# Kernel optimization log

Measured on AMD Instinct MI355X. Metric: run time of the kernel, lower is better.

The kernel has to match this reference:

```python
import jax, jax.numpy as jnp
import numpy as np

N_NODES = 100000
N_EDGES = 1600000
D_IN = 128
D_OUT = 128


def setup_inputs() -> dict:
    key = jax.random.key(0)
    ks = jax.random.split(key, 7)
    x = jax.random.normal(ks[0], (N_NODES, D_IN), dtype=jnp.float32)
    edge_index = jax.random.randint(ks[1], (2, N_EDGES), 0, N_NODES, dtype=jnp.int64)
    edge_weights = jax.random.uniform(ks[2], (N_EDGES,), dtype=jnp.float32)
    s = 1.0 / np.sqrt(D_IN)
    W_lin = jax.random.uniform(ks[3], (D_IN, D_OUT), minval=-s, maxval=s, dtype=jnp.float32)
    b_lin = jax.random.uniform(ks[4], (D_OUT,), minval=-s, maxval=s, dtype=jnp.float32)
    W_agg = jax.random.uniform(ks[5], (D_IN, D_OUT), minval=-s, maxval=s, dtype=jnp.float32)
    b_agg = jax.random.uniform(ks[6], (D_OUT,), minval=-s, maxval=s, dtype=jnp.float32)
    return {"x": x, "edge_index": edge_index, "edge_weights": edge_weights,
            "W_lin": W_lin, "b_lin": b_lin, "W_agg": W_agg, "b_agg": b_agg}


def reference(x, edge_index, edge_weights, W_lin, b_lin, W_agg, b_agg):
    # self transform: [N, D_out]
    self_features = x @ W_lin + b_lin
    row, col = edge_index[0], edge_index[1]
    # gather neighbor features along edges: [E, D_in]
    neighbor_features = x[col] * edge_weights[:, None]
    # per-edge transform: [E, D_out]
    msgs = neighbor_features @ W_agg + b_agg
    # scatter-add to destination nodes (index_add_ on row)
    aggregated = jax.ops.segment_sum(msgs, row, num_segments=x.shape[0])
    return self_features + aggregated
```

## Files before the change

kernel.cpp:

```cpp
#include <hip/hip_runtime.h>

#define N_NODES 100000
#define N_EDGES 1600000
#define D 128
#define SCAN_CHUNK 1024
#define NB_SCAN ((N_NODES + SCAN_CHUNK - 1) / SCAN_CHUNK)

#define BSHIFT 9
#define BUCK_NODES 512
#define NBUCK 196
#define SCAP 10240
#define PART_CHUNK 4096
#define PART_BLOCKS ((N_EDGES + PART_CHUNK - 1) / PART_CHUNK)
#define CONV_BLOCKS 6250
#define W_BLOCKS 128

typedef __attribute__((ext_vector_type(8))) short bf16x8;
typedef __attribute__((ext_vector_type(4))) float f32x4;
typedef __attribute__((ext_vector_type(4))) unsigned u32x4;

__device__ __forceinline__ unsigned bf16rne(float f) {
  unsigned u = __float_as_uint(f);
  return (u + 0x7fffu + ((u >> 16) & 1u)) >> 16;
}

#define T5_OFF    200
#define T5_FRAGW  100304
#define T5_SRT    116688
#define T5_XH     3316688
#define T5_ZH     9718736
#define WS_T5_BYTES ((size_t)16120784 * 4)

#define WS_OFF   100000
#define WS_BSUM  200004
#define WS_SRT   200192
#define WS_XH    3400192
#define WS_T1_BYTES ((size_t)3400192 * 4)
#define WS_T2_BYTES ((size_t)(3400192 + 6400000) * 4)

__global__ __launch_bounds__(256) void part_kernel(
    const int* __restrict__ ei, const float* __restrict__ ew,
    const float* __restrict__ x,
    const float* __restrict__ Wl, const float* __restrict__ Wa,
    int* __restrict__ pcur, int2* __restrict__ stage,
    uint4* __restrict__ xh4, unsigned short* __restrict__ fragW) {
  __shared__ int cntL[256];
  __shared__ int s0[256];
  __shared__ int gb[NBUCK];
  __shared__ int curL[NBUCK];
  __shared__ int2 recL[PART_CHUNK];
  __shared__ unsigned char buckL[PART_CHUNK];
  int bid = blockIdx.x, tid = threadIdx.x;

  if (bid < PART_BLOCKS) {
    cntL[tid] = 0;
    __syncthreads();
    int e0 = bid * PART_CHUNK;
    int tot = min(PART_CHUNK, N_EDGES - e0);
#pragma unroll
    for (int k = 0; k < PART_CHUNK / 256; k++) {
      int e = e0 + k * 256 + tid;
      if (e < N_EDGES) atomicAdd(&cntL[ei[e] >> BSHIFT], 1);
    }
    __syncthreads();
    s0[tid] = cntL[tid];
    __syncthreads();
    for (int o = 1; o < 256; o <<= 1) {
      int add = (tid >= o) ? s0[tid - o] : 0;
      __syncthreads();
      s0[tid] += add;
      __syncthreads();
    }
    if (tid < NBUCK) {
      gb[tid] = atomicAdd(&pcur[tid], cntL[tid]);
      curL[tid] = 0;
    }
    __syncthreads();
#pragma unroll
    for (int k = 0; k < PART_CHUNK / 256; k++) {
      int e = e0 + k * 256 + tid;
      if (e < N_EDGES) {
        int d = ei[e];
        int src = ei[N_EDGES + e];
        float w = ew[e];
        int b = d >> BSHIFT;
        int r = atomicAdd(&curL[b], 1);
        int slot = (s0[b] - cntL[b]) + r;
        recL[slot] = make_int2(src | ((d & (BUCK_NODES - 1)) << 17),
                               __float_as_int(w));
        buckL[slot] = (unsigned char)b;
      }
    }
    __syncthreads();
    for (int i = tid; i < tot; i += 256) {
      int b = buckL[i];
      int idx = gb[b] + (i - (s0[b] - cntL[b]));
      stage[(size_t)b * SCAP + idx] = recL[i];
    }
  } else if (bid < PART_BLOCKS + CONV_BLOCKS) {
    int g = (bid - PART_BLOCKS) * 256 + tid;
    const u32x4* xp = reinterpret_cast<const u32x4*>(x);
    u32x4 a = __builtin_nontemporal_load(xp + (size_t)g * 2);
    u32x4 b = __builtin_nontemporal_load(xp + (size_t)g * 2 + 1);
    uint4 o;
    o.x = bf16rne(__uint_as_float(a.x)) | (bf16rne(__uint_as_float(a.y)) << 16);
    o.y = bf16rne(__uint_as_float(a.z)) | (bf16rne(__uint_as_float(a.w)) << 16);
    o.z = bf16rne(__uint_as_float(b.x)) | (bf16rne(__uint_as_float(b.y)) << 16);
    o.w = bf16rne(__uint_as_float(b.z)) | (bf16rne(__uint_as_float(b.w)) << 16);
    xh4[g] = o;
  } else {
    int tau = (bid - PART_BLOCKS - CONV_BLOCKS) * 256 + tid;
    int slot = tau >> 3, j = tau & 7;
    int lane = slot & 63, ft = slot >> 6;
    int t = ft & 7, s = ft >> 3;
    int kl = (s & 3) * 32 + (lane >> 4) * 8 + j;
    int n = t * 16 + (lane & 15);
    float v = (s < 4 ? Wl : Wa)[kl * 128 + n];
    fragW[slot * 8 + j] = (unsigned short)bf16rne(v);
  }
}

__global__ __launch_bounds__(512) void binB2_kernel(const int* __restrict__ pcur,
                                                    const int2* __restrict__ stage,
                                                    int* __restrict__ off,
                                                    int2* __restrict__ srt) {
  __shared__ int pc[NBUCK];
  __shared__ int sa[BUCK_NODES];
  __shared__ int sb[BUCK_NODES];
  __shared__ int curL[BUCK_NODES];
  __shared__ int baseS, mS;
  int b = blockIdx.x, tid = threadIdx.x;
  if (tid < NBUCK) pc[tid] = pcur[tid];
  if (tid < BUCK_NODES) sa[tid] = 0;
  __syncthreads();
  if (tid == 0) {
    int s = 0;
    for (int i = 0; i < b; i++) s += pc[i];
    baseS = s;
    mS = pc[b];
  }
  __syncthreads();
  int base = baseS, m = mS;
  const int2* sp = stage + (size_t)b * SCAP;
  for (int r = tid; r < m; r += 512)
    atomicAdd(&sa[((unsigned)sp[r].x) >> 17], 1);
  __syncthreads();
  int* srcb = sa;
  int* dstb = sb;
  for (int o = 1; o < BUCK_NODES; o <<= 1) {
    if (tid < BUCK_NODES)
      dstb[tid] = srcb[tid] + (tid >= o ? srcb[tid - o] : 0);
    __syncthreads();
    int* t = srcb; srcb = dstb; dstb = t;
  }
  int nb = b << BSHIFT;
  int nn = min(BUCK_NODES, N_NODES - nb);
  if (tid < BUCK_NODES) {
    int ex = tid ? srcb[tid - 1] : 0;
    curL[tid] = ex;
    if (tid < nn) off[nb + tid] = base + ex;
  }
  if (tid == 0 && b == NBUCK - 1) off[N_NODES] = base + srcb[nn - 1];
  __syncthreads();
  for (int r = tid; r < m; r += 512) {
    int2 rec = sp[r];
    int ldst = ((unsigned)rec.x) >> 17;
    int s = atomicAdd(&curL[ldst], 1);
    srt[base + s] = make_int2(rec.x & 0x1FFFF, rec.y);
  }
}

#define FACC(s_, p_, w_)                                                    \
  {                                                                         \
    acc1[s_][0] = fmaf(w_, __uint_as_float((p_).x << 16), acc1[s_][0]);     \
    acc1[s_][1] = fmaf(w_, __uint_as_float((p_).x & 0xffff0000u), acc1[s_][1]); \
    acc1[s_][2] = fmaf(w_, __uint_as_float((p_).y << 16), acc1[s_][2]);     \
    acc1[s_][3] = fmaf(w_, __uint_as_float((p_).y & 0xffff0000u), acc1[s_][3]); \
    acc1[s_][4] = fmaf(w_, __uint_as_float((p_).z << 16), acc1[s_][4]);     \
    acc1[s_][5] = fmaf(w_, __uint_as_float((p_).z & 0xffff0000u), acc1[s_][5]); \
    acc1[s_][6] = fmaf(w_, __uint_as_float((p_).w << 16), acc1[s_][6]);     \
    acc1[s_][7] = fmaf(w_, __uint_as_float((p_).w & 0xffff0000u), acc1[s_][7]); \
  }

__global__ __launch_bounds__(256) void fused_gather_gemm_kernel(
    const uint4* __restrict__ xh4, const short* __restrict__ xh,
    const short* __restrict__ fragW, const int* __restrict__ off,
    const int2* __restrict__ srt,
    const float* __restrict__ bl, const float* __restrict__ ba,
    float* __restrict__ out) {
  int tid = threadIdx.x;
  int wave = tid >> 6, lane = tid & 63;
  int m = lane & 15, q = lane >> 4;
  int R = blockIdx.x * 64 + wave * 16;
  int n = R + m;

  float acc1[4][8];
#pragma unroll
  for (int s = 0; s < 4; s++)
#pragma unroll
    for (int j = 0; j < 8; j++) acc1[s][j] = 0.f;

  int beg = 0, end = 0;
  if (n < N_NODES) {
    beg = off[n];
    end = off[n + 1];
  }
  int e = beg;
  for (; e + 1 < end; e += 2) {
    int2 r0 = srt[e];
    int2 r1 = srt[e + 1];
    uint4 p00 = xh4[(size_t)r0.x * 16 + 0 * 4 + q];
    uint4 p01 = xh4[(size_t)r0.x * 16 + 1 * 4 + q];
    uint4 p02 = xh4[(size_t)r0.x * 16 + 2 * 4 + q];
    uint4 p03 = xh4[(size_t)r0.x * 16 + 3 * 4 + q];
    uint4 p10 = xh4[(size_t)r1.x * 16 + 0 * 4 + q];
    uint4 p11 = xh4[(size_t)r1.x * 16 + 1 * 4 + q];
    uint4 p12 = xh4[(size_t)r1.x * 16 + 2 * 4 + q];
    uint4 p13 = xh4[(size_t)r1.x * 16 + 3 * 4 + q];
    float w0 = __int_as_float(r0.y), w1 = __int_as_float(r1.y);
    FACC(0, p00, w0) FACC(1, p01, w0) FACC(2, p02, w0) FACC(3, p03, w0)
    FACC(0, p10, w1) FACC(1, p11, w1) FACC(2, p12, w1) FACC(3, p13, w1)
  }
  if (e < end) {
    int2 r0 = srt[e];
    uint4 p00 = xh4[(size_t)r0.x * 16 + 0 * 4 + q];
    uint4 p01 = xh4[(size_t)r0.x * 16 + 1 * 4 + q];
    uint4 p02 = xh4[(size_t)r0.x * 16 + 2 * 4 + q];
    uint4 p03 = xh4[(size_t)r0.x * 16 + 3 * 4 + q];
    float w0 = __int_as_float(r0.y);
    FACC(0, p00, w0) FACC(1, p01, w0) FACC(2, p02, w0) FACC(3, p03, w0)
  }

  bf16x8 az[4];
#pragma unroll
  for (int s = 0; s < 4; s++) {
    union { bf16x8 v; unsigned u[4]; } cv;
#pragma unroll
    for (int jj = 0; jj < 4; jj++)
      cv.u[jj] = bf16rne(acc1[s][2 * jj]) | (bf16rne(acc1[s][2 * jj + 1]) << 16);
    az[s] = cv.v;
  }

  const short* xrow = xh + (size_t)n * D + q * 8;
  const short* fw = fragW + (size_t)lane * 8;
  f32x4 acc[8];
#pragma unroll
  for (int t = 0; t < 8; t++) acc[t] = (f32x4){0.f, 0.f, 0.f, 0.f};

#pragma unroll
  for (int s = 0; s < 8; s++) {
    bf16x8 a;
    if (s < 4)
      a = *reinterpret_cast<const bf16x8*>(xrow + s * 32);
    else
      a = az[s - 4];
#pragma unroll
    for (int t = 0; t < 8; t++) {
      bf16x8 b = *reinterpret_cast<const bf16x8*>(fw + (size_t)((s * 8 + t) * 64) * 8);
      acc[t] = __builtin_amdgcn_mfma_f32_16x16x32_bf16(a, b, acc[t], 0, 0, 0);
    }
  }

  float blv[8], bav[8];
#pragma unroll
  for (int t = 0; t < 8; t++) {
    blv[t] = bl[t * 16 + m];
    bav[t] = ba[t * 16 + m];
  }
#pragma unroll
  for (int r = 0; r < 4; r++) {
    int row = R + q * 4 + r;
    if (row < N_NODES) {
      float dg = (float)(off[row + 1] - off[row]);
#pragma unroll
      for (int t = 0; t < 8; t++)
        __builtin_nontemporal_store(acc[t][r] + blv[t] + dg * bav[t],
                                    out + (size_t)row * D + t * 16 + m);
    }
  }
}


__global__ __launch_bounds__(256) void hist_kernel(const int* __restrict__ ei,
                                                   int* __restrict__ cnt) {
  int e = blockIdx.x * 256 + threadIdx.x;
  if (e < N_EDGES) atomicAdd(&cnt[ei[e]], 1);
}

__global__ __launch_bounds__(256) void block_sum_kernel(const int* __restrict__ cnt,
                                                        int* __restrict__ bsum) {
  int base = blockIdx.x * SCAN_CHUNK;
  int s = 0;
#pragma unroll
  for (int k = 0; k < 4; k++) {
    int i = base + (int)threadIdx.x + k * 256;
    if (i < N_NODES) s += cnt[i];
  }
  __shared__ int red[4];
  for (int o = 32; o > 0; o >>= 1) s += __shfl_down(s, o, 64);
  if ((threadIdx.x & 63) == 0) red[threadIdx.x >> 6] = s;
  __syncthreads();
  if (threadIdx.x == 0) bsum[blockIdx.x] = red[0] + red[1] + red[2] + red[3];
}

__global__ __launch_bounds__(128) void scan_bsum_kernel(int* __restrict__ bsum,
                                                        int* __restrict__ off) {
  __shared__ int sh[128];
  int t = threadIdx.x;
  int v = (t < NB_SCAN) ? bsum[t] : 0;
  sh[t] = v;
  __syncthreads();
  for (int o = 1; o < 128; o <<= 1) {
    int add = (t >= o) ? sh[t - o] : 0;
    __syncthreads();
    sh[t] += add;
    __syncthreads();
  }
  if (t < NB_SCAN) bsum[t] = sh[t] - v;
  if (t == 0) off[N_NODES] = sh[127];
}

__global__ __launch_bounds__(256) void scan_offsets_kernel(const int* __restrict__ cnt,
                                                           const int* __restrict__ bsum,
                                                           int* __restrict__ off) {
  __shared__ int sh[256];
  int t = threadIdx.x;
  int i0 = blockIdx.x * SCAN_CHUNK + t * 4;
  int c[4];
#pragma unroll
  for (int k = 0; k < 4; k++) c[k] = (i0 + k < N_NODES) ? cnt[i0 + k] : 0;
  int ls = c[0] + c[1] + c[2] + c[3];
  sh[t] = ls;
  __syncthreads();
  for (int o = 1; o < 256; o <<= 1) {
    int add = (t >= o) ? sh[t - o] : 0;
    __syncthreads();
    sh[t] += add;
    __syncthreads();
  }
  int run = bsum[blockIdx.x] + sh[t] - ls;
#pragma unroll
  for (int k = 0; k < 4; k++) {
    if (i0 + k < N_NODES) off[i0 + k] = run;
    run += c[k];
  }
}

__global__ __launch_bounds__(256) void fill_kernel(const int* __restrict__ ei,
                                                   const float* __restrict__ ew,
                                                   const int* __restrict__ off,
                                                   int* __restrict__ cur,
                                                   int2* __restrict__ srt) {
  int e = blockIdx.x * 256 + threadIdx.x;
  if (e >= N_EDGES) return;
  int dst = ei[e];
  int p = off[dst] + atomicAdd(&cur[dst], 1);
  srt[p] = make_int2(ei[N_EDGES + e], __float_as_int(ew[e]));
}

__global__ __launch_bounds__(256) void convert_kernel(const float* __restrict__ x,
                                                      uint4* __restrict__ xh) {
  int i = blockIdx.x * 256 + threadIdx.x;
  const float4* xp = reinterpret_cast<const float4*>(x);
  float4 a = xp[(size_t)i * 2];
  float4 b = xp[(size_t)i * 2 + 1];
  uint4 o;
  o.x = bf16rne(a.x) | (bf16rne(a.y) << 16);
  o.y = bf16rne(a.z) | (bf16rne(a.w) << 16);
  o.z = bf16rne(b.x) | (bf16rne(b.y) << 16);
  o.w = bf16rne(b.z) | (bf16rne(b.w) << 16);
  xh[i] = o;
}

__global__ __launch_bounds__(256) void gather_bf16_kernel(const unsigned* __restrict__ xh,
                                                          const int* __restrict__ off,
                                                          const int2* __restrict__ srt,
                                                          float* __restrict__ z,
                                                          float* __restrict__ degf) {
  int gid = blockIdx.x * 256 + threadIdx.x;
  int n = gid >> 5;
  int lane = gid & 31;
  if (n >= N_NODES) return;
  int beg = off[n], end = off[n + 1];
  float4 acc = make_float4(0.f, 0.f, 0.f, 0.f);
  int e = beg;
  for (; e + 1 < end; e += 2) {
    int2 r0 = srt[e];
    int2 r1 = srt[e + 1];
    uint2 p0 = *reinterpret_cast<const uint2*>(xh + (size_t)r0.x * 64 + lane * 2);
    uint2 p1 = *reinterpret_cast<const uint2*>(xh + (size_t)r1.x * 64 + lane * 2);
    float w0 = __int_as_float(r0.y);
    float w1 = __int_as_float(r1.y);
    acc.x = fmaf(w0, __uint_as_float(p0.x << 16), acc.x);
    acc.y = fmaf(w0, __uint_as_float(p0.x & 0xffff0000u), acc.y);
    acc.z = fmaf(w0, __uint_as_float(p0.y << 16), acc.z);
    acc.w = fmaf(w0, __uint_as_float(p0.y & 0xffff0000u), acc.w);
    acc.x = fmaf(w1, __uint_as_float(p1.x << 16), acc.x);
    acc.y = fmaf(w1, __uint_as_float(p1.x & 0xffff0000u), acc.y);
    acc.z = fmaf(w1, __uint_as_float(p1.y << 16), acc.z);
    acc.w = fmaf(w1, __uint_as_float(p1.y & 0xffff0000u), acc.w);
  }
  if (e < end) {
    int2 r0 = srt[e];
    uint2 p0 = *reinterpret_cast<const uint2*>(xh + (size_t)r0.x * 64 + lane * 2);
    float w0 = __int_as_float(r0.y);
    acc.x = fmaf(w0, __uint_as_float(p0.x << 16), acc.x);
    acc.y = fmaf(w0, __uint_as_float(p0.x & 0xffff0000u), acc.y);
    acc.z = fmaf(w0, __uint_as_float(p0.y << 16), acc.z);
    acc.w = fmaf(w0, __uint_as_float(p0.y & 0xffff0000u), acc.w);
  }
  *reinterpret_cast<float4*>(z + (size_t)n * D + (lane << 2)) = acc;
  if (lane == 0) degf[n] = (float)(end - beg);
}

__global__ __launch_bounds__(256) void gather_f32_kernel(const float* __restrict__ x,
                                                         const int* __restrict__ off,
                                                         const int2* __restrict__ srt,
                                                         float* __restrict__ z,
                                                         float* __restrict__ degf) {
  int gid = blockIdx.x * 256 + threadIdx.x;
  int n = gid >> 5;
  int lane = gid & 31;
  if (n >= N_NODES) return;
  int beg = off[n], end = off[n + 1];
  float4 acc = make_float4(0.f, 0.f, 0.f, 0.f);
  for (int e = beg; e < end; e++) {
    int2 r0 = srt[e];
    float4 x0 = *reinterpret_cast<const float4*>(x + (size_t)r0.x * D + (lane << 2));
    float w0 = __int_as_float(r0.y);
    acc.x = fmaf(w0, x0.x, acc.x); acc.y = fmaf(w0, x0.y, acc.y);
    acc.z = fmaf(w0, x0.z, acc.z); acc.w = fmaf(w0, x0.w, acc.w);
  }
  *reinterpret_cast<float4*>(z + (size_t)n * D + (lane << 2)) = acc;
  if (lane == 0) degf[n] = (float)(end - beg);
}

__global__ __launch_bounds__(256) void scatter_kernel(const float* __restrict__ x,
                                                      const int* __restrict__ ei,
                                                      const float* __restrict__ ew,
                                                      float* __restrict__ z,
                                                      float* __restrict__ deg) {
  long long g = (long long)blockIdx.x * 256 + threadIdx.x;
  int e = (int)(g >> 5);
  int lane = (int)(g & 31);
  if (e >= N_EDGES) return;
  int dst = ei[e];
  int src = ei[N_EDGES + e];
  float w = ew[e];
  float4 xv = *reinterpret_cast<const float4*>(x + (size_t)src * D + (lane << 2));
  float* o = z + (size_t)dst * D + (lane << 2);
  atomicAdd(o + 0, w * xv.x);
  atomicAdd(o + 1, w * xv.y);
  atomicAdd(o + 2, w * xv.z);
  atomicAdd(o + 3, w * xv.w);
  if (lane == 0) atomicAdd(deg + dst, 1.0f);
}

__global__ __launch_bounds__(256) void fused_gemm_kernel(const float* __restrict__ x,
                                                         const float* __restrict__ Wl,
                                                         const float* __restrict__ bl,
                                                         const float* __restrict__ Wa,
                                                         const float* __restrict__ ba,
                                                         const float* __restrict__ deg,
                                                         float* __restrict__ out) {
  __shared__ float xs[32 * 16];
  __shared__ float zs[32 * 16];
  __shared__ float wls[16 * 128];
  __shared__ float was[16 * 128];
  const int tid = threadIdx.x;
  const int row0 = blockIdx.x * 32;
  const int c4 = tid & 31;
  const int r0 = tid >> 5;
  float4 acc[4];
#pragma unroll
  for (int i = 0; i < 4; i++) acc[i] = make_float4(0.f, 0.f, 0.f, 0.f);

  for (int k0 = 0; k0 < D; k0 += 16) {
    {
      int t = tid & 127;
      int r = t >> 2;
      int kc = (t & 3) << 2;
      const float* sp = (tid < 128) ? x : out;
      float* dp = (tid < 128) ? xs : zs;
      *reinterpret_cast<float4*>(dp + r * 16 + kc) =
          *reinterpret_cast<const float4*>(sp + (size_t)(row0 + r) * D + k0 + kc);
    }
#pragma unroll
    for (int i = 0; i < 2; i++) {
      int f = tid + i * 256;
      int kk = f >> 5;
      int cc = (f & 31) << 2;
      *reinterpret_cast<float4*>(wls + kk * 128 + cc) =
          *reinterpret_cast<const float4*>(Wl + (size_t)(k0 + kk) * D + cc);
      *reinterpret_cast<float4*>(was + kk * 128 + cc) =
          *reinterpret_cast<const float4*>(Wa + (size_t)(k0 + kk) * D + cc);
    }
    __syncthreads();
#pragma unroll
    for (int kk = 0; kk < 16; kk++) {
      float4 wl = *reinterpret_cast<const float4*>(wls + kk * 128 + (c4 << 2));
      float4 wa = *reinterpret_cast<const float4*>(was + kk * 128 + (c4 << 2));
#pragma unroll
      for (int rr = 0; rr < 4; rr++) {
        int r2 = r0 + rr * 8;
        float xv = xs[r2 * 16 + kk];
        float zv = zs[r2 * 16 + kk];
        acc[rr].x = fmaf(xv, wl.x, fmaf(zv, wa.x, acc[rr].x));
        acc[rr].y = fmaf(xv, wl.y, fmaf(zv, wa.y, acc[rr].y));
        acc[rr].z = fmaf(xv, wl.z, fmaf(zv, wa.z, acc[rr].z));
        acc[rr].w = fmaf(xv, wl.w, fmaf(zv, wa.w, acc[rr].w));
      }
    }
    __syncthreads();
  }

  float4 blv = *reinterpret_cast<const float4*>(bl + (c4 << 2));
  float4 bav = *reinterpret_cast<const float4*>(ba + (c4 << 2));
#pragma unroll
  for (int rr = 0; rr < 4; rr++) {
    int r = row0 + r0 + rr * 8;
    float d = deg[r];
    float4 o;
    o.x = acc[rr].x + blv.x + d * bav.x;
    o.y = acc[rr].y + blv.y + d * bav.y;
    o.z = acc[rr].z + blv.z + d * bav.z;
    o.w = acc[rr].w + blv.w + d * bav.w;
    *reinterpret_cast<float4*>(out + (size_t)r * D + (c4 << 2)) = o;
  }
}

extern "C" void kernel_launch(void* const* d_in, const int* in_sizes, int n_in,
                              void* d_out, int out_size, void* d_ws, size_t ws_size,
                              hipStream_t stream) {
  const float* x  = (const float*)d_in[0];
  const int*   ei = (const int*)d_in[1];
  const float* ew = (const float*)d_in[2];
  const float* Wl = (const float*)d_in[3];
  const float* bl = (const float*)d_in[4];
  const float* Wa = (const float*)d_in[5];
  const float* ba = (const float*)d_in[6];
  float* out = (float*)d_out;

  if (ws_size >= WS_T5_BYTES) {
    int* pcur = (int*)d_ws;
    int* off = pcur + T5_OFF;
    unsigned short* fragW = (unsigned short*)(pcur + T5_FRAGW);
    int2* srt = (int2*)(pcur + T5_SRT);
    unsigned* xh = (unsigned*)(pcur + T5_XH);
    int2* stage = (int2*)(pcur + T5_ZH);

    hipMemsetAsync(pcur, 0, NBUCK * sizeof(int), stream);
    part_kernel<<<PART_BLOCKS + CONV_BLOCKS + W_BLOCKS, 256, 0, stream>>>(
        ei, ew, x, Wl, Wa, pcur, stage, (uint4*)xh, fragW);
    binB2_kernel<<<NBUCK, 512, 0, stream>>>(pcur, stage, off, srt);
    fused_gather_gemm_kernel<<<1563, 256, 0, stream>>>(
        (const uint4*)xh, (const short*)xh, (const short*)fragW, off, srt,
        bl, ba, out);
  } else if (ws_size >= WS_T1_BYTES) {
    int*  cnt  = (int*)d_ws;
    int*  off  = cnt + WS_OFF;
    int*  bsum = cnt + WS_BSUM;
    int2* srt  = (int2*)(cnt + WS_SRT);
    float* degf = (float*)cnt;

    hipMemsetAsync(cnt, 0, (size_t)N_NODES * sizeof(int), stream);
    hist_kernel<<<(N_EDGES + 255) / 256, 256, 0, stream>>>(ei, cnt);
    block_sum_kernel<<<NB_SCAN, 256, 0, stream>>>(cnt, bsum);
    scan_bsum_kernel<<<1, 128, 0, stream>>>(bsum, off);
    scan_offsets_kernel<<<NB_SCAN, 256, 0, stream>>>(cnt, bsum, off);
    hipMemsetAsync(cnt, 0, (size_t)N_NODES * sizeof(int), stream);
    fill_kernel<<<(N_EDGES + 255) / 256, 256, 0, stream>>>(ei, ew, off, cnt, srt);

    if (ws_size >= WS_T2_BYTES) {
      unsigned* xh = (unsigned*)(cnt + WS_XH);
      convert_kernel<<<(N_NODES * D / 8) / 256, 256, 0, stream>>>(x, (uint4*)xh);
      gather_bf16_kernel<<<(N_NODES * 32 + 255) / 256, 256, 0, stream>>>(xh, off, srt, out, degf);
    } else {
      gather_f32_kernel<<<(N_NODES * 32 + 255) / 256, 256, 0, stream>>>(x, off, srt, out, degf);
    }
    fused_gemm_kernel<<<N_NODES / 32, 256, 0, stream>>>(x, Wl, bl, Wa, ba, degf, out);
  } else {
    float* deg = (float*)d_ws;
    hipMemsetAsync(out, 0, (size_t)N_NODES * D * sizeof(float), stream);
    hipMemsetAsync(deg, 0, (size_t)N_NODES * sizeof(float), stream);
    scatter_kernel<<<(N_EDGES * 32) / 256, 256, 0, stream>>>(x, ei, ew, out, deg);
    fused_gemm_kernel<<<N_NODES / 32, 256, 0, stream>>>(x, Wl, bl, Wa, ba, deg, out);
  }
}
```

Before: 263.7 us.

## Move x/W bf16 conversion from partition kernel into bucket-sort kernel

The edge-partition kernel now handles only edge bucketing, at 512 threads per block. The x-to-bf16 conversion and W fragment packing move into the second kernel, where they run alongside the per-bucket sort blocks, now at 1024 threads per block. The intent is to overlap the bandwidth-heavy conversion with the small, latency-bound 196-block bucket sort rather than with the partition pass. In exchange, block sizes change and the sort blocks must share the GPU with many conversion blocks.

```diff
diff --git a/kernel.cpp b/kernel.cpp
--- a/kernel.cpp
+++ b/kernel.cpp
@@ -12,8 +12,8 @@
 #define SCAP 10240
 #define PART_CHUNK 4096
 #define PART_BLOCKS ((N_EDGES + PART_CHUNK - 1) / PART_CHUNK)
-#define CONV_BLOCKS 6250
-#define W_BLOCKS 128
+#define CONV2_BLOCKS 1563
+#define W2_BLOCKS 32
 
 typedef __attribute__((ext_vector_type(8))) short bf16x8;
 typedef __attribute__((ext_vector_type(4))) float f32x4;
@@ -38,12 +38,9 @@
 #define WS_T1_BYTES ((size_t)3400192 * 4)
 #define WS_T2_BYTES ((size_t)(3400192 + 6400000) * 4)
 
-__global__ __launch_bounds__(256) void part_kernel(
+__global__ __launch_bounds__(512) void part_edges_kernel(
     const int* __restrict__ ei, const float* __restrict__ ew,
-    const float* __restrict__ x,
-    const float* __restrict__ Wl, const float* __restrict__ Wa,
-    int* __restrict__ pcur, int2* __restrict__ stage,
-    uint4* __restrict__ xh4, unsigned short* __restrict__ fragW) {
+    int* __restrict__ pcur, int2* __restrict__ stage) {
   __shared__ int cntL[256];
   __shared__ int s0[256];
   __shared__ int gb[NBUCK];
@@ -52,64 +49,120 @@
   __shared__ unsigned char buckL[PART_CHUNK];
   int bid = blockIdx.x, tid = threadIdx.x;
 
-  if (bid < PART_BLOCKS) {
-    cntL[tid] = 0;
-    __syncthreads();
-    int e0 = bid * PART_CHUNK;
-    int tot = min(PART_CHUNK, N_EDGES - e0);
-#pragma unroll
-    for (int k = 0; k < PART_CHUNK / 256; k++) {
-      int e = e0 + k * 256 + tid;
-      if (e < N_EDGES) atomicAdd(&cntL[ei[e] >> BSHIFT], 1);
-    }
-    __syncthreads();
-    s0[tid] = cntL[tid];
-    __syncthreads();
-    for (int o = 1; o < 256; o <<= 1) {
-      int add = (tid >= o) ? s0[tid - o] : 0;
+  if (tid < 256) cntL[tid] = 0;
+  __syncthreads();
+  int e0 = bid * PART_CHUNK;
+  int tot = min(PART_CHUNK, N_EDGES - e0);
+#pragma unroll
+  for (int k = 0; k < PART_CHUNK / 512; k++) {
+    int e = e0 + k * 512 + tid;
+    if (e < N_EDGES) atomicAdd(&cntL[ei[e] >> BSHIFT], 1);
+  }
+  __syncthreads();
+  if (tid < 256) s0[tid] = cntL[tid];
+  __syncthreads();
+  for (int o = 1; o < 256; o <<= 1) {
+    int add = (tid < 256 && tid >= o) ? s0[tid - o] : 0;
+    __syncthreads();
+    if (tid < 256) s0[tid] += add;
+    __syncthreads();
+  }
+  if (tid < NBUCK) {
+    gb[tid] = atomicAdd(&pcur[tid], cntL[tid]);
+    curL[tid] = 0;
+  }
+  __syncthreads();
+#pragma unroll
+  for (int k = 0; k < PART_CHUNK / 512; k++) {
+    int e = e0 + k * 512 + tid;
+    if (e < N_EDGES) {
+      int d = ei[e];
+      int src = ei[N_EDGES + e];
+      float w = ew[e];
+      int b = d >> BSHIFT;
+      int r = atomicAdd(&curL[b], 1);
+      int slot = (s0[b] - cntL[b]) + r;
+      recL[slot] = make_int2(src | ((d & (BUCK_NODES - 1)) << 17),
+                             __float_as_int(w));
+      buckL[slot] = (unsigned char)b;
+    }
+  }
+  __syncthreads();
+  for (int i = tid; i < tot; i += 512) {
+    int b = buckL[i];
+    int idx = gb[b] + (i - (s0[b] - cntL[b]));
+    stage[(size_t)b * SCAP + idx] = recL[i];
+  }
+}
+
+__global__ __launch_bounds__(1024) void prep2_kernel(
+    const int* __restrict__ pcur, const int2* __restrict__ stage,
+    int* __restrict__ off, int2* __restrict__ srt,
+    const float* __restrict__ x, uint4* __restrict__ xh4,
+    const float* __restrict__ Wl, const float* __restrict__ Wa,
+    unsigned short* __restrict__ fragW) {
+  __shared__ int pc[NBUCK];
+  __shared__ int sa[BUCK_NODES];
+  __shared__ int sb[BUCK_NODES];
+  __shared__ int curL[BUCK_NODES];
+  __shared__ int baseS, mS;
+  int bid = blockIdx.x, tid = threadIdx.x;
+
+  if (bid < NBUCK) {
+    int b = bid;
+    if (tid < NBUCK) pc[tid] = pcur[tid];
+    if (tid < BUCK_NODES) sa[tid] = 0;
+    __syncthreads();
+    if (tid == 0) {
+      int s = 0;
+      for (int i = 0; i < b; i++) s += pc[i];
+      baseS = s;
+      mS = pc[b];
+    }
+    __syncthreads();
+    int base = baseS, m = mS;
+    const int2* sp = stage + (size_t)b * SCAP;
+    for (int r = tid; r < m; r += 1024)
+      atomicAdd(&sa[((unsigned)sp[r].x) >> 17], 1);
+    __syncthreads();
+    int* srcb = sa;
+    int* dstb = sb;
+    for (int o = 1; o < BUCK_NODES; o <<= 1) {
+      if (tid < BUCK_NODES)
+        dstb[tid] = srcb[tid] + (tid >= o ? srcb[tid - o] : 0);
       __syncthreads();
-      s0[tid] += add;
-      __syncthreads();
-    }
-    if (tid < NBUCK) {
-      gb[tid] = atomicAdd(&pcur[tid], cntL[tid]);
-      curL[tid] = 0;
-    }
-    __syncthreads();
-#pragma unroll
-    for (int k = 0; k < PART_CHUNK / 256; k++) {
-      int e = e0 + k * 256 + tid;
-      if (e < N_EDGES) {
-        int d = ei[e];
-        int src = ei[N_EDGES + e];
-        float w = ew[e];
-        int b = d >> BSHIFT;
-        int r = atomicAdd(&curL[b], 1);
-        int slot = (s0[b] - cntL[b]) + r;
-        recL[slot] = make_int2(src | ((d & (BUCK_NODES - 1)) << 17),
-                               __float_as_int(w));
-        buckL[slot] = (unsigned char)b;
-      }
-    }
-    __syncthreads();
-    for (int i = tid; i < tot; i += 256) {
-      int b = buckL[i];
-      int idx = gb[b] + (i - (s0[b] - cntL[b]));
-      stage[(size_t)b * SCAP + idx] = recL[i];
-    }
-  } else if (bid < PART_BLOCKS + CONV_BLOCKS) {
-    int g = (bid - PART_BLOCKS) * 256 + tid;
-    const u32x4* xp = reinterpret_cast<const u32x4*>(x);
-    u32x4 a = __builtin_nontemporal_load(xp + (size_t)g * 2);
-    u32x4 b = __builtin_nontemporal_load(xp + (size_t)g * 2 + 1);
-    uint4 o;
-    o.x = bf16rne(__uint_as_float(a.x)) | (bf16rne(__uint_as_float(a.y)) << 16);
-    o.y = bf16rne(__uint_as_float(a.z)) | (bf16rne(__uint_as_float(a.w)) << 16);
-    o.z = bf16rne(__uint_as_float(b.x)) | (bf16rne(__uint_as_float(b.y)) << 16);
-    o.w = bf16rne(__uint_as_float(b.z)) | (bf16rne(__uint_as_float(b.w)) << 16);
-    xh4[g] = o;
+      int* t = srcb; srcb = dstb; dstb = t;
+    }
+    int nb = b << BSHIFT;
+    int nn = min(BUCK_NODES, N_NODES - nb);
+    if (tid < BUCK_NODES) {
+      int ex = tid ? srcb[tid - 1] : 0;
+      curL[tid] = ex;
+      if (tid < nn) off[nb + tid] = base + ex;
+    }
+    if (tid == 0 && b == NBUCK - 1) off[N_NODES] = base + srcb[nn - 1];
+    __syncthreads();
+    for (int r = tid; r < m; r += 1024) {
+      int2 rec = sp[r];
+      int ldst = ((unsigned)rec.x) >> 17;
+      int s = atomicAdd(&curL[ldst], 1);
+      srt[base + s] = make_int2(rec.x & 0x1FFFF, rec.y);
+    }
+  } else if (bid < NBUCK + CONV2_BLOCKS) {
+    int g = (bid - NBUCK) * 1024 + tid;
+    if (g < N_NODES * D / 8) {
+      const u32x4* xp = reinterpret_cast<const u32x4*>(x);
+      u32x4 a = __builtin_nontemporal_load(xp + (size_t)g * 2);
+      u32x4 b = __builtin_nontemporal_load(xp + (size_t)g * 2 + 1);
+      uint4 o;
+      o.x = bf16rne(__uint_as_float(a.x)) | (bf16rne(__uint_as_float(a.y)) << 16);
+      o.y = bf16rne(__uint_as_float(a.z)) | (bf16rne(__uint_as_float(a.w)) << 16);
+      o.z = bf16rne(__uint_as_float(b.x)) | (bf16rne(__uint_as_float(b.y)) << 16);
+      o.w = bf16rne(__uint_as_float(b.z)) | (bf16rne(__uint_as_float(b.w)) << 16);
+      xh4[g] = o;
+    }
   } else {
-    int tau = (bid - PART_BLOCKS - CONV_BLOCKS) * 256 + tid;
+    int tau = (bid - NBUCK - CONV2_BLOCKS) * 1024 + tid;
     int slot = tau >> 3, j = tau & 7;
     int lane = slot & 63, ft = slot >> 6;
     int t = ft & 7, s = ft >> 3;
@@ -117,56 +170,6 @@
     int n = t * 16 + (lane & 15);
     float v = (s < 4 ? Wl : Wa)[kl * 128 + n];
     fragW[slot * 8 + j] = (unsigned short)bf16rne(v);
-  }
-}
-
-__global__ __launch_bounds__(512) void binB2_kernel(const int* __restrict__ pcur,
-                                                    const int2* __restrict__ stage,
-                                                    int* __restrict__ off,
-                                                    int2* __restrict__ srt) {
-  __shared__ int pc[NBUCK];
-  __shared__ int sa[BUCK_NODES];
-  __shared__ int sb[BUCK_NODES];
-  __shared__ int curL[BUCK_NODES];
-  __shared__ int baseS, mS;
-  int b = blockIdx.x, tid = threadIdx.x;
-  if (tid < NBUCK) pc[tid] = pcur[tid];
-  if (tid < BUCK_NODES) sa[tid] = 0;
-  __syncthreads();
-  if (tid == 0) {
-    int s = 0;
-    for (int i = 0; i < b; i++) s += pc[i];
-    baseS = s;
-    mS = pc[b];
-  }
-  __syncthreads();
-  int base = baseS, m = mS;
-  const int2* sp = stage + (size_t)b * SCAP;
-  for (int r = tid; r < m; r += 512)
-    atomicAdd(&sa[((unsigned)sp[r].x) >> 17], 1);
-  __syncthreads();
-  int* srcb = sa;
-  int* dstb = sb;
-  for (int o = 1; o < BUCK_NODES; o <<= 1) {
-    if (tid < BUCK_NODES)
-      dstb[tid] = srcb[tid] + (tid >= o ? srcb[tid - o] : 0);
-    __syncthreads();
-    int* t = srcb; srcb = dstb; dstb = t;
-  }
-  int nb = b << BSHIFT;
-  int nn = min(BUCK_NODES, N_NODES - nb);
-  if (tid < BUCK_NODES) {
-    int ex = tid ? srcb[tid - 1] : 0;
-    curL[tid] = ex;
-    if (tid < nn) off[nb + tid] = base + ex;
-  }
-  if (tid == 0 && b == NBUCK - 1) off[N_NODES] = base + srcb[nn - 1];
-  __syncthreads();
-  for (int r = tid; r < m; r += 512) {
-    int2 rec = sp[r];
-    int ldst = ((unsigned)rec.x) >> 17;
-    int s = atomicAdd(&curL[ldst], 1);
-    srt[base + s] = make_int2(rec.x & 0x1FFFF, rec.y);
   }
 }
 
@@ -550,9 +553,9 @@
     int2* stage = (int2*)(pcur + T5_ZH);
 
     hipMemsetAsync(pcur, 0, NBUCK * sizeof(int), stream);
-    part_kernel<<<PART_BLOCKS + CONV_BLOCKS + W_BLOCKS, 256, 0, stream>>>(
-        ei, ew, x, Wl, Wa, pcur, stage, (uint4*)xh, fragW);
-    binB2_kernel<<<NBUCK, 512, 0, stream>>>(pcur, stage, off, srt);
+    part_edges_kernel<<<PART_BLOCKS, 512, 0, stream>>>(ei, ew, pcur, stage);
+    prep2_kernel<<<NBUCK + CONV2_BLOCKS + W2_BLOCKS, 1024, 0, stream>>>(
+        pcur, stage, off, srt, x, (uint4*)xh, Wl, Wa, fragW);
     fused_gather_gemm_kernel<<<1563, 256, 0, stream>>>(
         (const uint4*)xh, (const short*)xh, (const short*)fragW, off, srt,
         bl, ba, out);
```

Result: no change. 265.4 us (+0.7%).

## Compute per-node offsets with global histogram and scan instead of per-bucket binning

Applied to the files above, without the earlier changes.

The partition kernel now also builds a global per-node degree histogram with global atomics. Offsets come from the existing three-kernel scan path rather than from a per-bucket shared-memory scan in binB2. binB2 shrinks to a pure scatter with 1024 threads and reads global offsets. The goal is to take the serial prefix loop and the local scan off the critical binning kernel, at the cost of 1.6M extra global atomics and three extra launches.

```diff
diff --git a/kernel.cpp b/kernel.cpp
--- a/kernel.cpp
+++ b/kernel.cpp
@@ -29,6 +29,9 @@
 #define T5_SRT    116688
 #define T5_XH     3316688
 #define T5_ZH     9718736
+#define T6_PCUR   13732816
+#define T6_CNT    13733012
+#define T6_BSUM   13833012
 #define WS_T5_BYTES ((size_t)16120784 * 4)
 
 #define WS_OFF   100000
@@ -42,7 +45,7 @@
     const int* __restrict__ ei, const float* __restrict__ ew,
     const float* __restrict__ x,
     const float* __restrict__ Wl, const float* __restrict__ Wa,
-    int* __restrict__ pcur, int2* __restrict__ stage,
+    int* __restrict__ pcur, int* __restrict__ cnt, int2* __restrict__ stage,
     uint4* __restrict__ xh4, unsigned short* __restrict__ fragW) {
   __shared__ int cntL[256];
   __shared__ int s0[256];
@@ -60,7 +63,11 @@
 #pragma unroll
     for (int k = 0; k < PART_CHUNK / 256; k++) {
       int e = e0 + k * 256 + tid;
-      if (e < N_EDGES) atomicAdd(&cntL[ei[e] >> BSHIFT], 1);
+      if (e < N_EDGES) {
+        int d = ei[e];
+        atomicAdd(&cntL[d >> BSHIFT], 1);
+        atomicAdd(&cnt[d], 1);
+      }
     }
     __syncthreads();
     s0[tid] = cntL[tid];
@@ -120,53 +127,22 @@
   }
 }
 
-__global__ __launch_bounds__(512) void binB2_kernel(const int* __restrict__ pcur,
-                                                    const int2* __restrict__ stage,
-                                                    int* __restrict__ off,
-                                                    int2* __restrict__ srt) {
-  __shared__ int pc[NBUCK];
-  __shared__ int sa[BUCK_NODES];
-  __shared__ int sb[BUCK_NODES];
+__global__ __launch_bounds__(1024) void binB2_kernel(const int* __restrict__ pcur,
+                                                     const int2* __restrict__ stage,
+                                                     const int* __restrict__ off,
+                                                     int2* __restrict__ srt) {
   __shared__ int curL[BUCK_NODES];
-  __shared__ int baseS, mS;
   int b = blockIdx.x, tid = threadIdx.x;
-  if (tid < NBUCK) pc[tid] = pcur[tid];
-  if (tid < BUCK_NODES) sa[tid] = 0;
+  if (tid < BUCK_NODES) curL[tid] = 0;
   __syncthreads();
-  if (tid == 0) {
-    int s = 0;
-    for (int i = 0; i < b; i++) s += pc[i];
-    baseS = s;
-    mS = pc[b];
-  }
-  __syncthreads();
-  int base = baseS, m = mS;
+  int m = pcur[b];
+  int nb = b << BSHIFT;
   const int2* sp = stage + (size_t)b * SCAP;
-  for (int r = tid; r < m; r += 512)
-    atomicAdd(&sa[((unsigned)sp[r].x) >> 17], 1);
-  __syncthreads();
-  int* srcb = sa;
-  int* dstb = sb;
-  for (int o = 1; o < BUCK_NODES; o <<= 1) {
-    if (tid < BUCK_NODES)
-      dstb[tid] = srcb[tid] + (tid >= o ? srcb[tid - o] : 0);
-    __syncthreads();
-    int* t = srcb; srcb = dstb; dstb = t;
-  }
-  int nb = b << BSHIFT;
-  int nn = min(BUCK_NODES, N_NODES - nb);
-  if (tid < BUCK_NODES) {
-    int ex = tid ? srcb[tid - 1] : 0;
-    curL[tid] = ex;
-    if (tid < nn) off[nb + tid] = base + ex;
-  }
-  if (tid == 0 && b == NBUCK - 1) off[N_NODES] = base + srcb[nn - 1];
-  __syncthreads();
-  for (int r = tid; r < m; r += 512) {
+  for (int r = tid; r < m; r += 1024) {
     int2 rec = sp[r];
     int ldst = ((unsigned)rec.x) >> 17;
     int s = atomicAdd(&curL[ldst], 1);
-    srt[base + s] = make_int2(rec.x & 0x1FFFF, rec.y);
+    srt[off[nb + ldst] + s] = make_int2(rec.x & 0x1FFFF, rec.y);
   }
 }
 
@@ -542,17 +518,23 @@
   float* out = (float*)d_out;
 
   if (ws_size >= WS_T5_BYTES) {
-    int* pcur = (int*)d_ws;
-    int* off = pcur + T5_OFF;
-    unsigned short* fragW = (unsigned short*)(pcur + T5_FRAGW);
-    int2* srt = (int2*)(pcur + T5_SRT);
-    unsigned* xh = (unsigned*)(pcur + T5_XH);
-    int2* stage = (int2*)(pcur + T5_ZH);
-
-    hipMemsetAsync(pcur, 0, NBUCK * sizeof(int), stream);
+    int* ws = (int*)d_ws;
+    int* off = ws + T5_OFF;
+    unsigned short* fragW = (unsigned short*)(ws + T5_FRAGW);
+    int2* srt = (int2*)(ws + T5_SRT);
+    unsigned* xh = (unsigned*)(ws + T5_XH);
+    int2* stage = (int2*)(ws + T5_ZH);
+    int* pcur = ws + T6_PCUR;
+    int* cnt = ws + T6_CNT;
+    int* bsum = ws + T6_BSUM;
+
+    hipMemsetAsync(pcur, 0, (NBUCK + N_NODES) * sizeof(int), stream);
     part_kernel<<<PART_BLOCKS + CONV_BLOCKS + W_BLOCKS, 256, 0, stream>>>(
-        ei, ew, x, Wl, Wa, pcur, stage, (uint4*)xh, fragW);
-    binB2_kernel<<<NBUCK, 512, 0, stream>>>(pcur, stage, off, srt);
+        ei, ew, x, Wl, Wa, pcur, cnt, stage, (uint4*)xh, fragW);
+    block_sum_kernel<<<NB_SCAN, 256, 0, stream>>>(cnt, bsum);
+    scan_bsum_kernel<<<1, 128, 0, stream>>>(bsum, off);
+    scan_offsets_kernel<<<NB_SCAN, 256, 0, stream>>>(cnt, bsum, off);
+    binB2_kernel<<<NBUCK, 1024, 0, stream>>>(pcur, stage, off, srt);
     fused_gather_gemm_kernel<<<1563, 256, 0, stream>>>(
         (const uint4*)xh, (const short*)xh, (const short*)fragW, off, srt,
         bl, ba, out);
```

New measurement: 319.6 us. 21.2% more time.
